# Performance work log

Hardware: AMD Instinct MI355X
Metric: run time of the kernel (lower is better)

## Reference

```python
import jax, jax.numpy as jnp
import numpy as np

H = 1024      # hidden_size
NH = 16       # num heads
HD = H // NH  # head dim


def setup_inputs() -> dict:
    key = jax.random.key(0)
    ks = jax.random.split(key, 10)
    s = 1.0 / np.sqrt(H)
    return {
        "hidden_states": jax.random.normal(ks[0], (2, 2048, H), jnp.float32),
        "attention_mask": jnp.zeros((2, 1, 1, 2048), jnp.float32),
        "Wq": jax.random.uniform(ks[1], (H, H), jnp.float32, -s, s),
        "bq": jnp.zeros((H,), jnp.float32),
        "Wk": jax.random.uniform(ks[2], (H, H), jnp.float32, -s, s),
        "bk": jnp.zeros((H,), jnp.float32),
        "Wv": jax.random.uniform(ks[3], (H, H), jnp.float32, -s, s),
        "bv": jnp.zeros((H,), jnp.float32),
        "Wo": jax.random.uniform(ks[4], (H, H), jnp.float32, -s, s),
        "bo": jnp.zeros((H,), jnp.float32),
    }


def _split_heads(x):
    b, s, _ = x.shape
    return x.reshape(b, s, NH, HD).transpose(0, 2, 1, 3)  # [B,NH,S,HD]


def reference(hidden_states, attention_mask, Wq, bq, Wk, bk, Wv, bv, Wo, bo):
    q = _split_heads(hidden_states @ Wq.T + bq)
    k = _split_heads(hidden_states @ Wk.T + bk)
    v = _split_heads(hidden_states @ Wv.T + bv)
    scores = jnp.einsum("bhqd,bhkd->bhqk", q, k) / np.sqrt(HD)
    scores = scores + attention_mask
    probs = jax.nn.softmax(scores, axis=-1)  # dropout prob=0 / eval mode -> no-op
    ctx = jnp.einsum("bhqk,bhkd->bhqd", probs, v)
    b, _, s, _ = ctx.shape
    ctx = ctx.transpose(0, 2, 1, 3).reshape(b, s, H)
    return ctx @ Wo.T + bo
```

## Files before the change

kernel.cpp:

```cpp
#include <hip/hip_runtime.h>
#include <hip/hip_bf16.h>

typedef __bf16 bf16_t;
typedef __bf16 bf16x8 __attribute__((ext_vector_type(8)));
typedef float f32x4 __attribute__((ext_vector_type(4)));
typedef float f32x16 __attribute__((ext_vector_type(16)));
typedef unsigned short u16;

#define DEVI __device__ __forceinline__
#define MFMA16x16x32(A, B, C) __builtin_amdgcn_mfma_f32_16x16x32_bf16(A, B, C, 0, 0, 0)
#define MFMA32x32x16(A, B, C) __builtin_amdgcn_mfma_f32_32x32x16_bf16(A, B, C, 0, 0, 0)

DEVI void gload_lds16(const void* g, void* l) {
  __builtin_amdgcn_global_load_lds(
      (const __attribute__((address_space(1))) void*)g,
      (__attribute__((address_space(3))) void*)l, 16, 0, 0);
}

DEVI u16 bits_of(bf16_t x) { return __builtin_bit_cast(u16, x); }

DEVI unsigned pk2(float lo, float hi) {
  return (unsigned)bits_of((bf16_t)lo) | ((unsigned)bits_of((bf16_t)hi) << 16);
}

DEVI bf16x8 mk_frag(unsigned s0, unsigned s1, unsigned s2, unsigned s3) {
  int4 t;
  t.x = (int)s0; t.y = (int)s1; t.z = (int)s2; t.w = (int)s3;
  return __builtin_bit_cast(bf16x8, t);
}

#if __has_builtin(__builtin_amdgcn_exp2f)
DEVI float exp2_fast(float x) { return __builtin_amdgcn_exp2f(x); }
#else
DEVI float exp2_fast(float x) { return __exp2f(x); }
#endif

__global__ void cvt_all(const float4* __restrict__ X,
                        const float4* __restrict__ Wq, const float4* __restrict__ Wk,
                        const float4* __restrict__ Wv, const float4* __restrict__ Wo,
                        ushort4* __restrict__ out) {
  int i = blockIdx.x * 256 + threadIdx.x;
  const float4* src;
  int off;
  if (i < 1048576) { src = X; off = i; }
  else {
    int j = i - 1048576;
    int seg = j >> 18;
    off = j & 262143;
    src = (seg == 0) ? Wq : (seg == 1) ? Wk : (seg == 2) ? Wv : Wo;
  }
  float4 v = src[off];
  ushort4 o;
  o.x = bits_of((bf16_t)v.x);
  o.y = bits_of((bf16_t)v.y);
  o.z = bits_of((bf16_t)v.z);
  o.w = bits_of((bf16_t)v.w);
  out[i] = o;
}

template <int OUT_KIND>
__global__ __launch_bounds__(256, 3) void gemm_bt(
    const bf16_t* __restrict__ A,
    const bf16_t* __restrict__ W0, const bf16_t* __restrict__ W1, const bf16_t* __restrict__ W2,
    const float* __restrict__ b0, const float* __restrict__ b1, const float* __restrict__ b2,
    void* o0, void* o1, void* o2, float s0, float s1, float s2) {
  constexpr int K = 1024, N = 1024;
  const int z = blockIdx.z;
  const bf16_t* W = (z == 0) ? W0 : ((z == 1) ? W1 : W2);
  const float* bias = (z == 0) ? b0 : ((z == 1) ? b1 : b2);
  void* out = (z == 0) ? o0 : ((z == 1) ? o1 : o2);
  const float scale = (z == 0) ? s0 : ((z == 1) ? s1 : s2);

  __shared__ bf16_t As[128 * 32];
  __shared__ bf16_t Bs[128 * 32];

  const int tid = threadIdx.x;
  const int wave = tid >> 6, lane = tid & 63;
  const int g = lane >> 4, l15 = lane & 15;
  const long m0 = (long)blockIdx.x * 128;
  const long n0 = (long)blockIdx.y * 128;

  const int srow = lane >> 2;
  const int scol = (lane & 3) * 8;

  const int wr = (wave >> 1) * 64;
  const int wc = (wave & 1) * 64;

  f32x4 acc[4][4] = {};

  for (int k0 = 0; k0 < K; k0 += 32) {
    __syncthreads();
#pragma unroll
    for (int t = 0; t < 2; ++t) {
      int chunk = wave * 2 + t;
      int row = chunk * 16 + srow;
      gload_lds16(A + (m0 + row) * K + k0 + scol, (char*)As + chunk * 1024);
      gload_lds16(W + (n0 + row) * K + k0 + scol, (char*)Bs + chunk * 1024);
    }
    __syncthreads();

    bf16x8 af[4], bfr[4];
#pragma unroll
    for (int i = 0; i < 4; ++i)
      af[i] = *(const bf16x8*)(As + (wr + i * 16 + l15) * 32 + g * 8);
#pragma unroll
    for (int i = 0; i < 4; ++i)
      bfr[i] = *(const bf16x8*)(Bs + (wc + i * 16 + l15) * 32 + g * 8);
    __builtin_amdgcn_s_setprio(1);
#pragma unroll
    for (int mi = 0; mi < 4; ++mi)
#pragma unroll
      for (int ni = 0; ni < 4; ++ni)
        acc[mi][ni] = MFMA16x16x32(af[mi], bfr[ni], acc[mi][ni]);
    __builtin_amdgcn_s_setprio(0);
  }

#pragma unroll
  for (int ni = 0; ni < 4; ++ni) {
    long col = n0 + wc + ni * 16 + l15;
    float bv = bias[col];
#pragma unroll
    for (int mi = 0; mi < 4; ++mi) {
#pragma unroll
      for (int r = 0; r < 4; ++r) {
        long row = m0 + wr + mi * 16 + g * 4 + r;
        float v = (acc[mi][ni][r] + bv) * scale;
        if (OUT_KIND == 0)
          ((bf16_t*)out)[row * N + col] = (bf16_t)v;
        else
          ((float*)out)[row * N + col] = v;
      }
    }
  }
}

__global__ __launch_bounds__(128, 2) void attn_fwd4(
    const bf16_t* __restrict__ Qm, const bf16_t* __restrict__ Km,
    const bf16_t* __restrict__ Vm, const float* __restrict__ mask,
    bf16_t* __restrict__ ctx) {
  constexpr int S = 2048, Hs = 1024;
  constexpr float L2E = 1.4426950408889634f;
  int id = blockIdx.y * 32 + blockIdx.x;
  int swz = ((id & 7) << 7) | (id >> 3);
  const int qb = swz & 31;
  const int bh = swz >> 5;
  const int b = bh >> 4, h = bh & 15;

  const int tid = threadIdx.x;
  const int wave = tid >> 6, lane = tid & 63;
  const int l31 = lane & 31, hi = lane >> 5;

  __shared__ bf16_t Kb_[2][64 * 64];
  __shared__ bf16_t Vb_[2][64 * 64];
  __shared__ float Ms[2048];

  const char* Kg = (const char*)(Km + ((long)b * S) * Hs + h * 64);
  const bf16_t* Vg = Vm + ((long)b * S) * Hs + h * 64;
  const float* mrow = mask + b * S;

  const long qrow = (long)b * S + qb * 64 + wave * 32 + l31;
  const bf16_t* Qr = Qm + qrow * Hs + h * 64 + hi * 8;
  bf16x8 qB[4];
#pragma unroll
  for (int ks = 0; ks < 4; ++ks) qB[ks] = *(const bf16x8*)(Qr + ks * 16);

  const int ka = tid & 15, dq = tid >> 4;
  const bf16_t* Vsrc0 = Vg + (long)(4 * ka) * Hs + dq * 8;

  const int krow_in8 = lane >> 3;
  const int kslot = (lane & 7) ^ krow_in8;

#pragma unroll
  for (int c = 0; c < 4; ++c) {
    int ch = wave * 4 + c;
    gload_lds16((const char*)mrow + ch * 1024 + lane * 16, (char*)Ms + ch * 1024);
  }
#pragma unroll
  for (int c = 0; c < 4; ++c) {
    int ch = wave * 4 + c;
    gload_lds16(Kg + (long)(ch * 8 + krow_in8) * (Hs * 2) + kslot * 16,
                (char*)Kb_[0] + ch * 1024);
  }
  int4 v0 = *(const int4*)(Vsrc0);
  int4 v1 = *(const int4*)(Vsrc0 + Hs);
  int4 v2 = *(const int4*)(Vsrc0 + 2 * Hs);
  int4 v3 = *(const int4*)(Vsrc0 + 3 * Hs);
  {
    const u16* p0 = (const u16*)&v0; const u16* p1 = (const u16*)&v1;
    const u16* p2 = (const u16*)&v2; const u16* p3 = (const u16*)&v3;
#pragma unroll
    for (int j = 0; j < 8; ++j) {
      int d = dq * 8 + j;
      int2 w;
      w.x = (int)((unsigned)p0[j] | ((unsigned)p1[j] << 16));
      w.y = (int)((unsigned)p2[j] | ((unsigned)p3[j] << 16));
      *(int2*)((char*)Vb_[0] + d * 128 + ((8 * ka) ^ (j << 4))) = w;
    }
  }
  __syncthreads();

  f32x16 acc0 = {}, acc1 = {};
  float rho = 0.0f, lrun = 0.0f;

  for (int t = 0; t < 32; ++t) {
    const int cur = t & 1;
    const char* kb_c = (const char*)Kb_[cur];
    const char* vb_c = (const char*)Vb_[cur];

    if (t < 31) {
      const bf16_t* Vs = Vsrc0 + (long)((t + 1) * 64) * Hs;
      v0 = *(const int4*)(Vs);
      v1 = *(const int4*)(Vs + Hs);
      v2 = *(const int4*)(Vs + 2 * Hs);
      v3 = *(const int4*)(Vs + 3 * Hs);
#pragma unroll
      for (int c = 0; c < 4; ++c) {
        int ch = wave * 4 + c;
        gload_lds16(Kg + (long)((t + 1) * 64 + ch * 8 + krow_in8) * (Hs * 2) + kslot * 16,
                    (char*)Kb_[cur ^ 1] + ch * 1024);
      }
    }
    const float* mbase = Ms + t * 64;
    float4 mk[8];
#pragma unroll
    for (int st = 0; st < 2; ++st)
#pragma unroll
      for (int rg = 0; rg < 4; ++rg)
        mk[st * 4 + rg] = *(const float4*)(mbase + st * 32 + rg * 8 + hi * 4);

    f32x16 sc0 = {}, sc1 = {};
    {
      bf16x8 kf0[4], kf1[4];
#pragma unroll
      for (int ks = 0; ks < 4; ++ks)
        kf0[ks] = *(const bf16x8*)(kb_c + l31 * 128 + (((2 * ks + hi) * 16) ^ ((l31 & 7) << 4)));
#pragma unroll
      for (int ks = 0; ks < 4; ++ks) {
        int row = 32 + l31;
        kf1[ks] = *(const bf16x8*)(kb_c + row * 128 + (((2 * ks + hi) * 16) ^ ((row & 7) << 4)));
      }
      __builtin_amdgcn_s_setprio(1);
#pragma unroll
      for (int ks = 0; ks < 4; ++ks) sc0 = MFMA32x32x16(kf0[ks], qB[ks], sc0);
#pragma unroll
      for (int ks = 0; ks < 4; ++ks) sc1 = MFMA32x32x16(kf1[ks], qB[ks], sc1);
      __builtin_amdgcn_s_setprio(0);
    }

    float m4[4] = {-1e30f, -1e30f, -1e30f, -1e30f};
#pragma unroll
    for (int st = 0; st < 2; ++st) {
      f32x16& s = st ? sc1 : sc0;
#pragma unroll
      for (int rg = 0; rg < 4; ++rg) {
        float4 m = mk[st * 4 + rg];
#pragma unroll
        for (int i = 0; i < 4; ++i) {
          float v = fmaf(((const float*)&m)[i], L2E, s[rg * 4 + i]);
          s[rg * 4 + i] = v;
          m4[i] = fmaxf(m4[i], v);
        }
      }
    }
    float mt = fmaxf(fmaxf(m4[0], m4[1]), fmaxf(m4[2], m4[3]));
    mt = fmaxf(mt, __shfl_xor(mt, 32, 64));

    if (!__all(mt - rho <= 24.0f)) {
      float mw = mt;
#pragma unroll
      for (int off = 1; off < 32; off <<= 1) mw = fmaxf(mw, __shfl_xor(mw, off, 64));
      float fct = exp2_fast(rho - mw);
      lrun *= fct;
#pragma unroll
      for (int i = 0; i < 16; ++i) { acc0[i] *= fct; acc1[i] *= fct; }
      rho = mw;
    }
    float rho_u = __builtin_amdgcn_readfirstlane(rho);
    if (rho_u != 0.0f) {
#pragma unroll
      for (int i = 0; i < 16; ++i) { sc0[i] -= rho_u; sc1[i] -= rho_u; }
    }

    float s4[4] = {0.f, 0.f, 0.f, 0.f};
#pragma unroll
    for (int st = 0; st < 2; ++st) {
      f32x16& s = st ? sc1 : sc0;
#pragma unroll
      for (int i = 0; i < 16; ++i) {
        float p = exp2_fast(s[i]);
        s[i] = p;
        s4[i & 3] += p;
      }
    }
    float ls = (s4[0] + s4[1]) + (s4[2] + s4[3]);
    ls += __shfl_xor(ls, 32, 64);
    lrun += ls;

    if (t < 31) {
      const u16* p0 = (const u16*)&v0; const u16* p1 = (const u16*)&v1;
      const u16* p2 = (const u16*)&v2; const u16* p3 = (const u16*)&v3;
      char* vb_n = (char*)Vb_[cur ^ 1];
#pragma unroll
      for (int j = 0; j < 8; ++j) {
        int d = dq * 8 + j;
        int2 w;
        w.x = (int)((unsigned)p0[j] | ((unsigned)p1[j] << 16));
        w.y = (int)((unsigned)p2[j] | ((unsigned)p3[j] << 16));
        *(int2*)(vb_n + d * 128 + ((8 * ka) ^ (j << 4))) = w;
      }
    }

#pragma unroll
    for (int st = 0; st < 2; ++st) {
      f32x16& s = st ? sc1 : sc0;
      unsigned a0 = pk2(s[0], s[1]),   b0 = pk2(s[4], s[5]);
      unsigned a1 = pk2(s[2], s[3]),   b1 = pk2(s[6], s[7]);
      unsigned a2 = pk2(s[8], s[9]),   b2 = pk2(s[12], s[13]);
      unsigned a3 = pk2(s[10], s[11]), b3 = pk2(s[14], s[15]);
      asm("v_permlane32_swap_b32 %0, %1" : "+v"(a0), "+v"(b0));
      asm("v_permlane32_swap_b32 %0, %1" : "+v"(a1), "+v"(b1));
      asm("v_permlane32_swap_b32 %0, %1" : "+v"(a2), "+v"(b2));
      asm("v_permlane32_swap_b32 %0, %1" : "+v"(a3), "+v"(b3));
      bf16x8 pb0 = mk_frag(a0, a1, b0, b1);
      bf16x8 pb1 = mk_frag(a2, a3, b2, b3);
#pragma unroll
      for (int ks2 = 0; ks2 < 2; ++ks2) {
        bf16x8 pb = ks2 ? pb1 : pb0;
        int slot = st * 4 + ks2 * 2 + hi;
        bf16x8 va0 = *(const bf16x8*)(vb_c + l31 * 128 + ((slot * 16) ^ ((l31 & 7) << 4)));
        int d1 = 32 + l31;
        bf16x8 va1 = *(const bf16x8*)(vb_c + d1 * 128 + ((slot * 16) ^ ((d1 & 7) << 4)));
        __builtin_amdgcn_s_setprio(1);
        acc0 = MFMA32x32x16(va0, pb, acc0);
        acc1 = MFMA32x32x16(va1, pb, acc1);
        __builtin_amdgcn_s_setprio(0);
      }
    }
    __syncthreads();
  }

  float inv = 1.0f / lrun;
  bf16_t* cb = ctx + qrow * Hs + h * 64;
#pragma unroll
  for (int dh = 0; dh < 2; ++dh) {
    f32x16& a = dh ? acc1 : acc0;
#pragma unroll
    for (int rg = 0; rg < 4; ++rg) {
      ushort4 o;
      o.x = bits_of((bf16_t)(a[rg * 4 + 0] * inv));
      o.y = bits_of((bf16_t)(a[rg * 4 + 1] * inv));
      o.z = bits_of((bf16_t)(a[rg * 4 + 2] * inv));
      o.w = bits_of((bf16_t)(a[rg * 4 + 3] * inv));
      *(ushort4*)(cb + dh * 32 + rg * 8 + hi * 4) = o;
    }
  }
}

extern "C" void kernel_launch(void* const* d_in, const int* in_sizes, int n_in,
                              void* d_out, int out_size, void* d_ws, size_t ws_size,
                              hipStream_t stream) {
  (void)in_sizes; (void)n_in; (void)out_size; (void)ws_size;
  const float* X  = (const float*)d_in[0];
  const float* mask = (const float*)d_in[1];
  const float* Wq = (const float*)d_in[2];
  const float* bq = (const float*)d_in[3];
  const float* Wk = (const float*)d_in[4];
  const float* bk = (const float*)d_in[5];
  const float* Wv = (const float*)d_in[6];
  const float* bv = (const float*)d_in[7];
  const float* Wo = (const float*)d_in[8];
  const float* bo = (const float*)d_in[9];

  char* ws = (char*)d_ws;
  bf16_t* Xb  = (bf16_t*)(ws + 0);
  bf16_t* Wqb = (bf16_t*)(ws + 8388608);
  bf16_t* Wkb = (bf16_t*)(ws + 10485760);
  bf16_t* Wvb = (bf16_t*)(ws + 12582912);
  bf16_t* Wob = (bf16_t*)(ws + 14680064);
  bf16_t* Qb  = (bf16_t*)(ws + 16777216);
  bf16_t* Kb  = (bf16_t*)(ws + 25165824);
  bf16_t* Vb  = (bf16_t*)(ws + 33554432);
  bf16_t* Cb  = (bf16_t*)(ws + 41943040);

  cvt_all<<<8192, 256, 0, stream>>>((const float4*)X, (const float4*)Wq, (const float4*)Wk,
                                    (const float4*)Wv, (const float4*)Wo, (ushort4*)Xb);

  const float QSCALE = 0.125f * 1.4426950408889634f;
  dim3 gq(32, 8, 3);
  gemm_bt<0><<<gq, 256, 0, stream>>>(Xb, Wqb, Wkb, Wvb, bq, bk, bv, Qb, Kb, Vb,
                                     QSCALE, 1.0f, 1.0f);

  dim3 ga(32, 32, 1);
  attn_fwd4<<<ga, 128, 0, stream>>>(Qb, Kb, Vb, mask, Cb);

  dim3 go(32, 8, 1);
  gemm_bt<1><<<go, 256, 0, stream>>>(Cb, Wob, Wob, Wob, bo, bo, bo, d_out, d_out, d_out,
                                     1.0f, 1.0f, 1.0f);
}
```

Measured before the change: 130.1 us.

## Software-pipeline PV MFMAs one tile behind QK in attention loop

The attention kernel now defers the P·V MFMAs of each key tile to the next iteration. Those MFMAs are issued right after the next tile's QK^T MFMAs and before the softmax, so matrix work can overlap the exp/max arithmetic. V fragments and the packed P fragments are carried across iterations in registers, and a final drain after the loop handles the last tile. K fragment loads are hoisted to the top of the iteration, and the V-to-LDS transpose store moves to after P packing. This costs extra VGPRs for the carried fragments, which could raise register pressure at the 2-blocks-per-CU launch bound.

```diff
diff --git a/kernel.cpp b/kernel.cpp
--- a/kernel.cpp
+++ b/kernel.cpp
@@ -134,7 +134,7 @@
   }
 }
 
-__global__ __launch_bounds__(128, 2) void attn_fwd4(
+__global__ __launch_bounds__(128, 2) void attn_fwd5(
     const bf16_t* __restrict__ Qm, const bf16_t* __restrict__ Km,
     const bf16_t* __restrict__ Vm, const float* __restrict__ mask,
     bf16_t* __restrict__ ctx) {
@@ -201,11 +201,23 @@
 
   f32x16 acc0 = {}, acc1 = {};
   float rho = 0.0f, lrun = 0.0f;
+  bf16x8 pbP[4] = {};
+  bf16x8 vaP[8] = {};
 
   for (int t = 0; t < 32; ++t) {
     const int cur = t & 1;
     const char* kb_c = (const char*)Kb_[cur];
     const char* vb_c = (const char*)Vb_[cur];
+
+    bf16x8 kf0[4], kf1[4];
+#pragma unroll
+    for (int ks = 0; ks < 4; ++ks)
+      kf0[ks] = *(const bf16x8*)(kb_c + l31 * 128 + (((2 * ks + hi) * 16) ^ ((l31 & 7) << 4)));
+#pragma unroll
+    for (int ks = 0; ks < 4; ++ks) {
+      int row = 32 + l31;
+      kf1[ks] = *(const bf16x8*)(kb_c + row * 128 + (((2 * ks + hi) * 16) ^ ((row & 7) << 4)));
+    }
 
     if (t < 31) {
       const bf16_t* Vs = Vsrc0 + (long)((t + 1) * 64) * Hs;
@@ -229,23 +241,36 @@
         mk[st * 4 + rg] = *(const float4*)(mbase + st * 32 + rg * 8 + hi * 4);
 
     f32x16 sc0 = {}, sc1 = {};
-    {
-      bf16x8 kf0[4], kf1[4];
-#pragma unroll
-      for (int ks = 0; ks < 4; ++ks)
-        kf0[ks] = *(const bf16x8*)(kb_c + l31 * 128 + (((2 * ks + hi) * 16) ^ ((l31 & 7) << 4)));
-#pragma unroll
-      for (int ks = 0; ks < 4; ++ks) {
-        int row = 32 + l31;
-        kf1[ks] = *(const bf16x8*)(kb_c + row * 128 + (((2 * ks + hi) * 16) ^ ((row & 7) << 4)));
-      }
+    __builtin_amdgcn_s_setprio(1);
+#pragma unroll
+    for (int ks = 0; ks < 4; ++ks) sc0 = MFMA32x32x16(kf0[ks], qB[ks], sc0);
+#pragma unroll
+    for (int ks = 0; ks < 4; ++ks) sc1 = MFMA32x32x16(kf1[ks], qB[ks], sc1);
+    __builtin_amdgcn_s_setprio(0);
+
+    if (t > 0) {
       __builtin_amdgcn_s_setprio(1);
 #pragma unroll
-      for (int ks = 0; ks < 4; ++ks) sc0 = MFMA32x32x16(kf0[ks], qB[ks], sc0);
-#pragma unroll
-      for (int ks = 0; ks < 4; ++ks) sc1 = MFMA32x32x16(kf1[ks], qB[ks], sc1);
+      for (int st = 0; st < 2; ++st)
+#pragma unroll
+        for (int ks2 = 0; ks2 < 2; ++ks2) {
+          int i = st * 2 + ks2;
+          acc0 = MFMA32x32x16(vaP[i * 2 + 0], pbP[i], acc0);
+          acc1 = MFMA32x32x16(vaP[i * 2 + 1], pbP[i], acc1);
+        }
       __builtin_amdgcn_s_setprio(0);
     }
+
+#pragma unroll
+    for (int st = 0; st < 2; ++st)
+#pragma unroll
+      for (int ks2 = 0; ks2 < 2; ++ks2) {
+        int slot = st * 4 + ks2 * 2 + hi;
+        int i = st * 2 + ks2;
+        vaP[i * 2 + 0] = *(const bf16x8*)(vb_c + l31 * 128 + ((slot * 16) ^ ((l31 & 7) << 4)));
+        int d1 = 32 + l31;
+        vaP[i * 2 + 1] = *(const bf16x8*)(vb_c + d1 * 128 + ((slot * 16) ^ ((d1 & 7) << 4)));
+      }
 
     float m4[4] = {-1e30f, -1e30f, -1e30f, -1e30f};
 #pragma unroll
@@ -295,20 +320,6 @@
     float ls = (s4[0] + s4[1]) + (s4[2] + s4[3]);
     ls += __shfl_xor(ls, 32, 64);
     lrun += ls;
-
-    if (t < 31) {
-      const u16* p0 = (const u16*)&v0; const u16* p1 = (const u16*)&v1;
-      const u16* p2 = (const u16*)&v2; const u16* p3 = (const u16*)&v3;
-      char* vb_n = (char*)Vb_[cur ^ 1];
-#pragma unroll
-      for (int j = 0; j < 8; ++j) {
-        int d = dq * 8 + j;
-        int2 w;
-        w.x = (int)((unsigned)p0[j] | ((unsigned)p1[j] << 16));
-        w.y = (int)((unsigned)p2[j] | ((unsigned)p3[j] << 16));
-        *(int2*)(vb_n + d * 128 + ((8 * ka) ^ (j << 4))) = w;
-      }
-    }
 
 #pragma unroll
     for (int st = 0; st < 2; ++st) {
@@ -321,23 +332,36 @@
       asm("v_permlane32_swap_b32 %0, %1" : "+v"(a1), "+v"(b1));
       asm("v_permlane32_swap_b32 %0, %1" : "+v"(a2), "+v"(b2));
       asm("v_permlane32_swap_b32 %0, %1" : "+v"(a3), "+v"(b3));
-      bf16x8 pb0 = mk_frag(a0, a1, b0, b1);
-      bf16x8 pb1 = mk_frag(a2, a3, b2, b3);
-#pragma unroll
-      for (int ks2 = 0; ks2 < 2; ++ks2) {
-        bf16x8 pb = ks2 ? pb1 : pb0;
-        int slot = st * 4 + ks2 * 2 + hi;
-        bf16x8 va0 = *(const bf16x8*)(vb_c + l31 * 128 + ((slot * 16) ^ ((l31 & 7) << 4)));
-        int d1 = 32 + l31;
-        bf16x8 va1 = *(const bf16x8*)(vb_c + d1 * 128 + ((slot * 16) ^ ((d1 & 7) << 4)));
-        __builtin_amdgcn_s_setprio(1);
-        acc0 = MFMA32x32x16(va0, pb, acc0);
-        acc1 = MFMA32x32x16(va1, pb, acc1);
-        __builtin_amdgcn_s_setprio(0);
+      pbP[st * 2 + 0] = mk_frag(a0, a1, b0, b1);
+      pbP[st * 2 + 1] = mk_frag(a2, a3, b2, b3);
+    }
+
+    if (t < 31) {
+      const u16* p0 = (const u16*)&v0; const u16* p1 = (const u16*)&v1;
+      const u16* p2 = (const u16*)&v2; const u16* p3 = (const u16*)&v3;
+      char* vb_n = (char*)Vb_[cur ^ 1];
+#pragma unroll
+      for (int j = 0; j < 8; ++j) {
+        int d = dq * 8 + j;
+        int2 w;
+        w.x = (int)((unsigned)p0[j] | ((unsigned)p1[j] << 16));
+        w.y = (int)((unsigned)p2[j] | ((unsigned)p3[j] << 16));
+        *(int2*)(vb_n + d * 128 + ((8 * ka) ^ (j << 4))) = w;
       }
     }
     __syncthreads();
   }
+
+  __builtin_amdgcn_s_setprio(1);
+#pragma unroll
+  for (int st = 0; st < 2; ++st)
+#pragma unroll
+    for (int ks2 = 0; ks2 < 2; ++ks2) {
+      int i = st * 2 + ks2;
+      acc0 = MFMA32x32x16(vaP[i * 2 + 0], pbP[i], acc0);
+      acc1 = MFMA32x32x16(vaP[i * 2 + 1], pbP[i], acc1);
+    }
+  __builtin_amdgcn_s_setprio(0);
 
   float inv = 1.0f / lrun;
   bf16_t* cb = ctx + qrow * Hs + h * 64;
@@ -391,7 +415,7 @@
                                      QSCALE, 1.0f, 1.0f);
 
   dim3 ga(32, 32, 1);
-  attn_fwd4<<<ga, 128, 0, stream>>>(Qb, Kb, Vb, mask, Cb);
+  attn_fwd5<<<ga, 128, 0, stream>>>(Qb, Kb, Vb, mask, Cb);
 
   dim3 go(32, 8, 1);
   gemm_bt<1><<<go, 256, 0, stream>>>(Cb, Wob, Wob, Wob, bo, bo, bo, d_out, d_out, d_out,
```

New measurement: 128.8 us. Within noise of the previous version (-1.1%).

## Load K fragments directly into registers and software-pipeline PV MFMAs across tiles

Applied to the files above, without the earlier changes.

The attention kernel stops staging K through LDS. Each lane now loads its K fragments straight from global memory into double-buffered registers, prefetched one tile ahead. The P·V MFMAs for tile t are deferred and issued right after the QK MFMAs of tile t+1, so matrix work can overlap the softmax math. The V LDS layout also gets an extra XOR swizzle bit to cut bank conflicts. In exchange, register pressure rises considerably (K fragments, V fragments and P fragments are all held live), which at launch bounds of 2 may cause spills. The K loads also become uncoalesced per-lane global reads.

```diff
diff --git a/kernel.cpp b/kernel.cpp
--- a/kernel.cpp
+++ b/kernel.cpp
@@ -134,7 +134,7 @@
   }
 }
 
-__global__ __launch_bounds__(128, 2) void attn_fwd4(
+__global__ __launch_bounds__(128, 2) void attn_fwd6(
     const bf16_t* __restrict__ Qm, const bf16_t* __restrict__ Km,
     const bf16_t* __restrict__ Vm, const float* __restrict__ mask,
     bf16_t* __restrict__ ctx) {
@@ -150,11 +150,9 @@
   const int wave = tid >> 6, lane = tid & 63;
   const int l31 = lane & 31, hi = lane >> 5;
 
-  __shared__ bf16_t Kb_[2][64 * 64];
   __shared__ bf16_t Vb_[2][64 * 64];
   __shared__ float Ms[2048];
 
-  const char* Kg = (const char*)(Km + ((long)b * S) * Hs + h * 64);
   const bf16_t* Vg = Vm + ((long)b * S) * Hs + h * 64;
   const float* mrow = mask + b * S;
 
@@ -164,22 +162,15 @@
 #pragma unroll
   for (int ks = 0; ks < 4; ++ks) qB[ks] = *(const bf16x8*)(Qr + ks * 16);
 
+  const bf16_t* Klane = Km + ((long)b * S) * Hs + h * 64 + (long)l31 * Hs + hi * 8;
+
   const int ka = tid & 15, dq = tid >> 4;
   const bf16_t* Vsrc0 = Vg + (long)(4 * ka) * Hs + dq * 8;
-
-  const int krow_in8 = lane >> 3;
-  const int kslot = (lane & 7) ^ krow_in8;
 
 #pragma unroll
   for (int c = 0; c < 4; ++c) {
     int ch = wave * 4 + c;
     gload_lds16((const char*)mrow + ch * 1024 + lane * 16, (char*)Ms + ch * 1024);
-  }
-#pragma unroll
-  for (int c = 0; c < 4; ++c) {
-    int ch = wave * 4 + c;
-    gload_lds16(Kg + (long)(ch * 8 + krow_in8) * (Hs * 2) + kslot * 16,
-                (char*)Kb_[0] + ch * 1024);
   }
   int4 v0 = *(const int4*)(Vsrc0);
   int4 v1 = *(const int4*)(Vsrc0 + Hs);
@@ -194,150 +185,174 @@
       int2 w;
       w.x = (int)((unsigned)p0[j] | ((unsigned)p1[j] << 16));
       w.y = (int)((unsigned)p2[j] | ((unsigned)p3[j] << 16));
-      *(int2*)((char*)Vb_[0] + d * 128 + ((8 * ka) ^ (j << 4))) = w;
+      *(int2*)((char*)Vb_[0] + d * 128 + ((8 * ka) ^ (j << 4) ^ ((dq & 1) << 5))) = w;
     }
   }
+  bf16x8 kfA[8], kfB[8];
+#pragma unroll
+  for (int st = 0; st < 2; ++st)
+#pragma unroll
+    for (int ks = 0; ks < 4; ++ks)
+      kfA[st * 4 + ks] = *(const bf16x8*)(Klane + (long)(st * 32) * Hs + ks * 16);
   __syncthreads();
 
   f32x16 acc0 = {}, acc1 = {};
   float rho = 0.0f, lrun = 0.0f;
-
-  for (int t = 0; t < 32; ++t) {
-    const int cur = t & 1;
-    const char* kb_c = (const char*)Kb_[cur];
-    const char* vb_c = (const char*)Vb_[cur];
-
-    if (t < 31) {
-      const bf16_t* Vs = Vsrc0 + (long)((t + 1) * 64) * Hs;
-      v0 = *(const int4*)(Vs);
-      v1 = *(const int4*)(Vs + Hs);
-      v2 = *(const int4*)(Vs + 2 * Hs);
-      v3 = *(const int4*)(Vs + 3 * Hs);
-#pragma unroll
-      for (int c = 0; c < 4; ++c) {
-        int ch = wave * 4 + c;
-        gload_lds16(Kg + (long)((t + 1) * 64 + ch * 8 + krow_in8) * (Hs * 2) + kslot * 16,
-                    (char*)Kb_[cur ^ 1] + ch * 1024);
-      }
-    }
-    const float* mbase = Ms + t * 64;
-    float4 mk[8];
-#pragma unroll
-    for (int st = 0; st < 2; ++st)
-#pragma unroll
-      for (int rg = 0; rg < 4; ++rg)
-        mk[st * 4 + rg] = *(const float4*)(mbase + st * 32 + rg * 8 + hi * 4);
-
-    f32x16 sc0 = {}, sc1 = {};
-    {
-      bf16x8 kf0[4], kf1[4];
-#pragma unroll
-      for (int ks = 0; ks < 4; ++ks)
-        kf0[ks] = *(const bf16x8*)(kb_c + l31 * 128 + (((2 * ks + hi) * 16) ^ ((l31 & 7) << 4)));
-#pragma unroll
-      for (int ks = 0; ks < 4; ++ks) {
-        int row = 32 + l31;
-        kf1[ks] = *(const bf16x8*)(kb_c + row * 128 + (((2 * ks + hi) * 16) ^ ((row & 7) << 4)));
-      }
-      __builtin_amdgcn_s_setprio(1);
-#pragma unroll
-      for (int ks = 0; ks < 4; ++ks) sc0 = MFMA32x32x16(kf0[ks], qB[ks], sc0);
-#pragma unroll
-      for (int ks = 0; ks < 4; ++ks) sc1 = MFMA32x32x16(kf1[ks], qB[ks], sc1);
-      __builtin_amdgcn_s_setprio(0);
-    }
-
-    float m4[4] = {-1e30f, -1e30f, -1e30f, -1e30f};
-#pragma unroll
-    for (int st = 0; st < 2; ++st) {
-      f32x16& s = st ? sc1 : sc0;
-#pragma unroll
-      for (int rg = 0; rg < 4; ++rg) {
-        float4 m = mk[st * 4 + rg];
-#pragma unroll
-        for (int i = 0; i < 4; ++i) {
-          float v = fmaf(((const float*)&m)[i], L2E, s[rg * 4 + i]);
-          s[rg * 4 + i] = v;
-          m4[i] = fmaxf(m4[i], v);
-        }
-      }
-    }
-    float mt = fmaxf(fmaxf(m4[0], m4[1]), fmaxf(m4[2], m4[3]));
-    mt = fmaxf(mt, __shfl_xor(mt, 32, 64));
-
-    if (!__all(mt - rho <= 24.0f)) {
-      float mw = mt;
-#pragma unroll
-      for (int off = 1; off < 32; off <<= 1) mw = fmaxf(mw, __shfl_xor(mw, off, 64));
-      float fct = exp2_fast(rho - mw);
-      lrun *= fct;
-#pragma unroll
-      for (int i = 0; i < 16; ++i) { acc0[i] *= fct; acc1[i] *= fct; }
-      rho = mw;
-    }
-    float rho_u = __builtin_amdgcn_readfirstlane(rho);
-    if (rho_u != 0.0f) {
-#pragma unroll
-      for (int i = 0; i < 16; ++i) { sc0[i] -= rho_u; sc1[i] -= rho_u; }
-    }
-
-    float s4[4] = {0.f, 0.f, 0.f, 0.f};
-#pragma unroll
-    for (int st = 0; st < 2; ++st) {
-      f32x16& s = st ? sc1 : sc0;
-#pragma unroll
-      for (int i = 0; i < 16; ++i) {
-        float p = exp2_fast(s[i]);
-        s[i] = p;
-        s4[i & 3] += p;
-      }
-    }
-    float ls = (s4[0] + s4[1]) + (s4[2] + s4[3]);
-    ls += __shfl_xor(ls, 32, 64);
-    lrun += ls;
-
-    if (t < 31) {
-      const u16* p0 = (const u16*)&v0; const u16* p1 = (const u16*)&v1;
-      const u16* p2 = (const u16*)&v2; const u16* p3 = (const u16*)&v3;
-      char* vb_n = (char*)Vb_[cur ^ 1];
-#pragma unroll
-      for (int j = 0; j < 8; ++j) {
-        int d = dq * 8 + j;
-        int2 w;
-        w.x = (int)((unsigned)p0[j] | ((unsigned)p1[j] << 16));
-        w.y = (int)((unsigned)p2[j] | ((unsigned)p3[j] << 16));
-        *(int2*)(vb_n + d * 128 + ((8 * ka) ^ (j << 4))) = w;
-      }
-    }
-
-#pragma unroll
-    for (int st = 0; st < 2; ++st) {
-      f32x16& s = st ? sc1 : sc0;
-      unsigned a0 = pk2(s[0], s[1]),   b0 = pk2(s[4], s[5]);
-      unsigned a1 = pk2(s[2], s[3]),   b1 = pk2(s[6], s[7]);
-      unsigned a2 = pk2(s[8], s[9]),   b2 = pk2(s[12], s[13]);
-      unsigned a3 = pk2(s[10], s[11]), b3 = pk2(s[14], s[15]);
-      asm("v_permlane32_swap_b32 %0, %1" : "+v"(a0), "+v"(b0));
-      asm("v_permlane32_swap_b32 %0, %1" : "+v"(a1), "+v"(b1));
-      asm("v_permlane32_swap_b32 %0, %1" : "+v"(a2), "+v"(b2));
-      asm("v_permlane32_swap_b32 %0, %1" : "+v"(a3), "+v"(b3));
-      bf16x8 pb0 = mk_frag(a0, a1, b0, b1);
-      bf16x8 pb1 = mk_frag(a2, a3, b2, b3);
-#pragma unroll
-      for (int ks2 = 0; ks2 < 2; ++ks2) {
-        bf16x8 pb = ks2 ? pb1 : pb0;
-        int slot = st * 4 + ks2 * 2 + hi;
-        bf16x8 va0 = *(const bf16x8*)(vb_c + l31 * 128 + ((slot * 16) ^ ((l31 & 7) << 4)));
-        int d1 = 32 + l31;
-        bf16x8 va1 = *(const bf16x8*)(vb_c + d1 * 128 + ((slot * 16) ^ ((d1 & 7) << 4)));
-        __builtin_amdgcn_s_setprio(1);
-        acc0 = MFMA32x32x16(va0, pb, acc0);
-        acc1 = MFMA32x32x16(va1, pb, acc1);
-        __builtin_amdgcn_s_setprio(0);
-      }
-    }
-    __syncthreads();
-  }
+  bf16x8 pbP[4] = {};
+  bf16x8 vaP[8] = {};
+
+#define ATTN_TILE(T, KC, KN)                                                        \
+  {                                                                                 \
+    const int cur = (T) & 1;                                                        \
+    const char* vb_c = (const char*)Vb_[cur];                                       \
+                  \
+    if ((T) < 31) {                                                                 \
+      const bf16_t* Vs = Vsrc0 + (long)(((T) + 1) * 64) * Hs;                       \
+      v0 = *(const int4*)(Vs);                                                      \
+      v1 = *(const int4*)(Vs + Hs);                                                 \
+      v2 = *(const int4*)(Vs + 2 * Hs);                                             \
+      v3 = *(const int4*)(Vs + 3 * Hs);                                             \
+      const bf16_t* Kt = Klane + (long)(((T) + 1) * 64) * Hs;                       \
+      _Pragma("unroll")                                                             \
+      for (int st = 0; st < 2; ++st) {                                              \
+        _Pragma("unroll")                                                           \
+        for (int ks = 0; ks < 4; ++ks)                                              \
+          KN[st * 4 + ks] = *(const bf16x8*)(Kt + (long)(st * 32) * Hs + ks * 16);  \
+      }                                                                             \
+    }                                                                               \
+    const float* mbase = Ms + (T) * 64;                                             \
+    float4 mk[8];                                                                   \
+    _Pragma("unroll")                                                               \
+    for (int st = 0; st < 2; ++st) {                                                \
+      _Pragma("unroll")                                                             \
+      for (int rg = 0; rg < 4; ++rg)                                                \
+        mk[st * 4 + rg] = *(const float4*)(mbase + st * 32 + rg * 8 + hi * 4);      \
+    }                                                                               \
+                                                            \
+    f32x16 sc0 = {}, sc1 = {};                                                      \
+    __builtin_amdgcn_s_setprio(1);                                                  \
+    _Pragma("unroll")                                                               \
+    for (int ks = 0; ks < 4; ++ks) sc0 = MFMA32x32x16(KC[ks], qB[ks], sc0);         \
+    _Pragma("unroll")                                                               \
+    for (int ks = 0; ks < 4; ++ks) sc1 = MFMA32x32x16(KC[4 + ks], qB[ks], sc1);     \
+    __builtin_amdgcn_s_setprio(0);                                                  \
+                                \
+    if ((T) > 0) {                                                                  \
+      __builtin_amdgcn_s_setprio(1);                                                \
+      _Pragma("unroll")                                                             \
+      for (int i5 = 0; i5 < 4; ++i5) {                                              \
+        acc0 = MFMA32x32x16(vaP[i5 * 2 + 0], pbP[i5], acc0);                        \
+        acc1 = MFMA32x32x16(vaP[i5 * 2 + 1], pbP[i5], acc1);                        \
+      }                                                                             \
+      __builtin_amdgcn_s_setprio(0);                                                \
+    }                                                                               \
+                                 \
+    _Pragma("unroll")                                                               \
+    for (int st = 0; st < 2; ++st) {                                                \
+      _Pragma("unroll")                                                             \
+      for (int ks2 = 0; ks2 < 2; ++ks2) {                                           \
+        int slot = st * 4 + ks2 * 2 + hi;                                           \
+        int i5 = st * 2 + ks2;                                                      \
+        int d0 = l31, d1 = 32 + l31;                                                \
+        vaP[i5 * 2 + 0] = *(const bf16x8*)(vb_c + d0 * 128 +                        \
+            ((slot * 16) ^ ((d0 & 7) << 4) ^ (((d0 >> 3) & 1) << 5)));              \
+        vaP[i5 * 2 + 1] = *(const bf16x8*)(vb_c + d1 * 128 +                        \
+            ((slot * 16) ^ ((d1 & 7) << 4) ^ (((d1 >> 3) & 1) << 5)));              \
+      }                                                                             \
+    }                                                                               \
+                            \
+    float m4[4] = {-1e30f, -1e30f, -1e30f, -1e30f};                                 \
+    _Pragma("unroll")                                                               \
+    for (int st = 0; st < 2; ++st) {                                                \
+      f32x16& s = st ? sc1 : sc0;                                                   \
+      _Pragma("unroll")                                                             \
+      for (int rg = 0; rg < 4; ++rg) {                                              \
+        float4 m = mk[st * 4 + rg];                                                 \
+        _Pragma("unroll")                                                           \
+        for (int i5 = 0; i5 < 4; ++i5) {                                            \
+          float v = fmaf(((const float*)&m)[i5], L2E, s[rg * 4 + i5]);              \
+          s[rg * 4 + i5] = v;                                                       \
+          m4[i5] = fmaxf(m4[i5], v);                                                \
+        }                                                                           \
+      }                                                                             \
+    }                                                                               \
+    float mt = fmaxf(fmaxf(m4[0], m4[1]), fmaxf(m4[2], m4[3]));                     \
+    mt = fmaxf(mt, __shfl_xor(mt, 32, 64));                                         \
+    if (!__all(mt - rho <= 24.0f)) {                                                \
+      float mw = mt;                                                                \
+      _Pragma("unroll")                                                             \
+      for (int off = 1; off < 32; off <<= 1) mw = fmaxf(mw, __shfl_xor(mw, off, 64));\
+      float fct = exp2_fast(rho - mw);                                              \
+      lrun *= fct;                                                                  \
+      _Pragma("unroll")                                                             \
+      for (int i5 = 0; i5 < 16; ++i5) { acc0[i5] *= fct; acc1[i5] *= fct; }         \
+      rho = mw;                                                                     \
+    }                                                                               \
+    float rho_u = __builtin_amdgcn_readfirstlane(rho);                              \
+    if (rho_u != 0.0f) {                                                            \
+      _Pragma("unroll")                                                             \
+      for (int i5 = 0; i5 < 16; ++i5) { sc0[i5] -= rho_u; sc1[i5] -= rho_u; }       \
+    }                                                                               \
+    float s4[4] = {0.f, 0.f, 0.f, 0.f};                                             \
+    _Pragma("unroll")                                                               \
+    for (int st = 0; st < 2; ++st) {                                                \
+      f32x16& s = st ? sc1 : sc0;                                                   \
+      _Pragma("unroll")                                                             \
+      for (int i5 = 0; i5 < 16; ++i5) {                                             \
+        float p = exp2_fast(s[i5]);                                                 \
+        s[i5] = p;                                                                  \
+        s4[i5 & 3] += p;                                                            \
+      }                                                                             \
+    }                                                                               \
+    float ls = (s4[0] + s4[1]) + (s4[2] + s4[3]);                                   \
+    ls += __shfl_xor(ls, 32, 64);                                                   \
+    lrun += ls;                                                                     \
+                                    \
+    _Pragma("unroll")                                                               \
+    for (int st = 0; st < 2; ++st) {                                                \
+      f32x16& s = st ? sc1 : sc0;                                                   \
+      unsigned a0 = pk2(s[0], s[1]),   c0 = pk2(s[4], s[5]);                        \
+      unsigned a1 = pk2(s[2], s[3]),   c1 = pk2(s[6], s[7]);                        \
+      unsigned a2 = pk2(s[8], s[9]),   c2 = pk2(s[12], s[13]);                      \
+      unsigned a3 = pk2(s[10], s[11]), c3 = pk2(s[14], s[15]);                      \
+      asm("v_permlane32_swap_b32 %0, %1" : "+v"(a0), "+v"(c0));                     \
+      asm("v_permlane32_swap_b32 %0, %1" : "+v"(a1), "+v"(c1));                     \
+      asm("v_permlane32_swap_b32 %0, %1" : "+v"(a2), "+v"(c2));                     \
+      asm("v_permlane32_swap_b32 %0, %1" : "+v"(a3), "+v"(c3));                     \
+      pbP[st * 2 + 0] = mk_frag(a0, a1, c0, c1);                                    \
+      pbP[st * 2 + 1] = mk_frag(a2, a3, c2, c3);                                    \
+    }                                                                               \
+                                                             \
+    if ((T) < 31) {                                                                 \
+      const u16* p0 = (const u16*)&v0; const u16* p1 = (const u16*)&v1;             \
+      const u16* p2 = (const u16*)&v2; const u16* p3 = (const u16*)&v3;             \
+      char* vb_n = (char*)Vb_[cur ^ 1];                                             \
+      _Pragma("unroll")                                                             \
+      for (int j = 0; j < 8; ++j) {                                                 \
+        int d = dq * 8 + j;                                                         \
+        int2 w;                                                                     \
+        w.x = (int)((unsigned)p0[j] | ((unsigned)p1[j] << 16));                     \
+        w.y = (int)((unsigned)p2[j] | ((unsigned)p3[j] << 16));                     \
+        *(int2*)(vb_n + d * 128 + ((8 * ka) ^ (j << 4) ^ ((dq & 1) << 5))) = w;     \
+      }                                                                             \
+    }                                                                               \
+    __syncthreads();                                                                \
+  }
+
+  for (int tt = 0; tt < 16; ++tt) {
+    int t0 = 2 * tt;
+    ATTN_TILE(t0, kfA, kfB);
+    ATTN_TILE((t0 + 1), kfB, kfA);
+  }
+#undef ATTN_TILE
+
+  __builtin_amdgcn_s_setprio(1);
+#pragma unroll
+  for (int i5 = 0; i5 < 4; ++i5) {
+    acc0 = MFMA32x32x16(vaP[i5 * 2 + 0], pbP[i5], acc0);
+    acc1 = MFMA32x32x16(vaP[i5 * 2 + 1], pbP[i5], acc1);
+  }
+  __builtin_amdgcn_s_setprio(0);
 
   float inv = 1.0f / lrun;
   bf16_t* cb = ctx + qrow * Hs + h * 64;
@@ -391,7 +406,7 @@
                                      QSCALE, 1.0f, 1.0f);
 
   dim3 ga(32, 32, 1);
-  attn_fwd4<<<ga, 128, 0, stream>>>(Qb, Kb, Vb, mask, Cb);
+  attn_fwd6<<<ga, 128, 0, stream>>>(Qb, Kb, Vb, mask, Cb);
 
   dim3 go(32, 8, 1);
   gemm_bt<1><<<go, 256, 0, stream>>>(Cb, Wob, Wob, Wob, bo, bo, bo, d_out, d_out, d_out,
```

After: 173.5 us. 1.33x slower.
